# Kernel tuning notes

Measured on AMD Instinct MI355X. Metric: run time of the kernel, lower is better.

The kernel has to match this reference:

```python
import jax, jax.numpy as jnp
import numpy as np
from jax import lax

D_MODEL = 1024
D_STATE = 128
D_CONV = 4
EXPAND = 2
HEADDIM = 64
D_INNER = EXPAND * D_MODEL          # 2048
NHEADS = D_INNER // HEADDIM         # 32
D_IN_PROJ = 2 * D_INNER + 2 * D_STATE + NHEADS  # 4384 (z, xBC, dt)
CONV_CH = D_INNER + 2 * D_STATE     # 2304
CHUNK = 128
EPS = 1e-5
BATCH, SEQ = 2, 2048


def silu(x):
    return x * jax.nn.sigmoid(x)


def rmsnorm(x, w):
    return x * lax.rsqrt(jnp.mean(x * x, axis=-1, keepdims=True) + EPS) * w


def segsum(a):
    # a: (b,h,c,q) -> (b,h,c,q,q); [i,j] = sum_{j<k<=i} a_k, -inf above diag
    q = a.shape[-1]
    cs = jnp.cumsum(a, axis=-1)
    seg = cs[..., :, None] - cs[..., None, :]
    mask = jnp.tril(jnp.ones((q, q), dtype=bool))
    return jnp.where(mask, seg, -jnp.inf)


def ssd(xh, dt, A, B, C):
    # xh: (b,l,h,p), dt: (b,l,h), A: (h,), B,C: (b,l,n). Chunked SSD scan.
    b, l, h, p = xh.shape
    n = B.shape[-1]
    c = l // CHUNK
    X = (xh * dt[..., None]).reshape(b, c, CHUNK, h, p)
    Adt = (A * dt).reshape(b, c, CHUNK, h).transpose(0, 3, 1, 2)  # (b,h,c,q)
    Bc = B.reshape(b, c, CHUNK, n)
    Cc = C.reshape(b, c, CHUNK, n)
    Acs = jnp.cumsum(Adt, axis=-1)
    L = jnp.exp(segsum(Adt))  # (b,h,c,q,q) causal decay within chunk
    Y_diag = jnp.einsum('bcln,bcsn,bhcls,bcshp->bclhp', Cc, Bc, L, X)
    decay_states = jnp.exp(Acs[..., -1:] - Acs)
    states = jnp.einsum('bcln,bhcl,bclhp->bchpn', Bc, decay_states, X)
    chunk_decay = jnp.exp(Acs[..., -1])  # (b,h,c)

    def step(s, inp):
        st, cd = inp
        return s * cd[:, :, None, None] + st, s

    init = jnp.zeros((b, h, p, n), dtype=xh.dtype)
    _, prev = lax.scan(step, init,
                       (states.transpose(1, 0, 2, 3, 4), chunk_decay.transpose(2, 0, 1)))
    # prev: (c,b,h,p,n) = state at start of each chunk
    Y_off = jnp.einsum('bcln,cbhpn,bhcl->bclhp', Cc, prev, jnp.exp(Acs))
    return (Y_diag + Y_off).reshape(b, l, h, p)


def mamba2(x, in_w, conv_w, conv_b, dt_bias, A_log, D, gnorm_w, out_w):
    b, l, _ = x.shape
    zxbcdt = x @ in_w.T  # (b,l,D_IN_PROJ)
    z = zxbcdt[..., :D_INNER]
    xBC = zxbcdt[..., D_INNER:D_INNER + CONV_CH]
    dt = jax.nn.softplus(zxbcdt[..., D_INNER + CONV_CH:] + dt_bias)  # (b,l,h)
    # causal depthwise conv1d
    xp = jnp.pad(xBC, ((0, 0), (D_CONV - 1, 0), (0, 0)))
    conv = sum(xp[:, k:k + l, :] * conv_w[:, k] for k in range(D_CONV)) + conv_b
    xBC = silu(conv)
    xs = xBC[..., :D_INNER]
    B = xBC[..., D_INNER:D_INNER + D_STATE]
    C = xBC[..., D_INNER + D_STATE:]
    A = -jnp.exp(A_log)
    xh = xs.reshape(b, l, NHEADS, HEADDIM)
    y = ssd(xh, dt, A, B, C) + xh * D[None, None, :, None]
    y = y.reshape(b, l, D_INNER)
    y = rmsnorm(y * silu(z), gnorm_w)  # RMSNormGated
    return y @ out_w.T


def setup_inputs() -> dict:
    key = jax.random.key(0)
    ks = jax.random.split(key, 24)
    d = {}
    d['x'] = jax.random.normal(ks[0], (BATCH, SEQ, D_MODEL), dtype=jnp.float32)
    d['norm_w'] = jnp.ones((D_MODEL,), jnp.float32)
    d['out_w_blk'] = jax.random.normal(ks[1], (D_MODEL, 2 * D_MODEL), jnp.float32) * 0.02
    d['out_b_blk'] = jnp.zeros((D_MODEL,), jnp.float32)
    for i, pfx in enumerate(['f_', 'b_']):
        o = 2 + i * 10
        d[pfx + 'in_w'] = jax.random.normal(ks[o], (D_IN_PROJ, D_MODEL), jnp.float32) * 0.02
        d[pfx + 'conv_w'] = jax.random.normal(ks[o + 1], (CONV_CH, D_CONV), jnp.float32) * 0.2
        d[pfx + 'conv_b'] = jnp.zeros((CONV_CH,), jnp.float32)
        d[pfx + 'dt_bias'] = jax.random.normal(ks[o + 2], (NHEADS,), jnp.float32) * 0.1
        d[pfx + 'A_log'] = jnp.log(jax.random.uniform(ks[o + 3], (NHEADS,), jnp.float32, 1.0, 16.0))
        d[pfx + 'D'] = jnp.ones((NHEADS,), jnp.float32)
        d[pfx + 'gnorm_w'] = jnp.ones((D_INNER,), jnp.float32)
        d[pfx + 'out_w'] = jax.random.normal(ks[o + 4], (D_MODEL, D_INNER), jnp.float32) * 0.02
    return d


def reference(x, norm_w, out_w_blk, out_b_blk,
              f_in_w, f_conv_w, f_conv_b, f_dt_bias, f_A_log, f_D, f_gnorm_w, f_out_w,
              b_in_w, b_conv_w, b_conv_b, b_dt_bias, b_A_log, b_D, b_gnorm_w, b_out_w):
    xn = rmsnorm(x, norm_w)
    y_fwd = mamba2(xn, f_in_w, f_conv_w, f_conv_b, f_dt_bias, f_A_log, f_D, f_gnorm_w, f_out_w)
    y_bwd = jnp.flip(
        mamba2(jnp.flip(xn, axis=1), b_in_w, b_conv_w, b_conv_b, b_dt_bias, b_A_log, b_D, b_gnorm_w, b_out_w),
        axis=1)
    out = jnp.concatenate([y_fwd, y_bwd], axis=-1) @ out_w_blk.T + out_b_blk
    return x + out
```

## Files before the change

kernel.cpp:

```cpp
#include <hip/hip_runtime.h>
#include <hip/hip_bf16.h>
#include <math.h>

#define BATCH 2
#define SEQL 2048
#define T 4096
#define DMODEL 1024
#define DINNER 2048
#define DSTATE 128
#define NH 32
#define HD 64
#define DPROJ2 4352
#define CONVCH 2304
#define NCH 16
#define CHUNK 128
#define EPS 1e-5f

#define N_INW ((size_t)DPROJ2 * DMODEL)
#define N_OUTW ((size_t)DMODEL * DINNER)
#define N_ST ((size_t)BATCH * NCH * NH * HD * DSTATE)
#define F2B_BLOCKS 10752
#define TW_BLOCKS 1024

typedef unsigned short u16;
typedef __bf16 bf16x8 __attribute__((ext_vector_type(8)));
typedef float f32x4 __attribute__((ext_vector_type(4)));

__device__ __forceinline__ u16 f2b(float f) {
    union { float f; unsigned u; } v; v.f = f;
    unsigned r = v.u + 0x7fffu + ((v.u >> 16) & 1u);
    return (u16)(r >> 16);
}
__device__ __forceinline__ float b2f(u16 b) {
    union { unsigned u; float f; } v; v.u = ((unsigned)b) << 16;
    return v.f;
}
__device__ __forceinline__ int flipseq(int r) {
    return (r & ~(SEQL - 1)) | ((SEQL - 1) - (r & (SEQL - 1)));
}
__device__ __forceinline__ void gload16(const u16* g, u16* l) {
    __builtin_amdgcn_global_load_lds(
        (const __attribute__((address_space(1))) void*)g,
        (__attribute__((address_space(3))) void*)l, 16, 0, 0);
}

__device__ __forceinline__ float blockReduceSum(float v) {
    __shared__ float red_[4];
    for (int off = 32; off > 0; off >>= 1) v += __shfl_down(v, off);
    int lane = threadIdx.x & 63, wid = threadIdx.x >> 6;
    if (lane == 0) red_[wid] = v;
    __syncthreads();
    if (threadIdx.x == 0) {
        float s = 0.f;
        int nw = blockDim.x >> 6;
        for (int i = 0; i < nw; ++i) s += red_[i];
        red_[0] = s;
    }
    __syncthreads();
    return red_[0];
}

__global__ __launch_bounds__(256) void k_rmsnorm(
    const float* __restrict__ x, const float* __restrict__ w,
    u16* __restrict__ outb)
{
    int row = blockIdx.x;
    const float* xr = x + (size_t)row * DMODEL;
    float ss = 0.f;
    for (int i = threadIdx.x; i < DMODEL; i += 256) { float v = xr[i]; ss += v * v; }
    float tot = blockReduceSum(ss);
    float sc = rsqrtf(tot / DMODEL + EPS);
    for (int i = threadIdx.x; i < DMODEL; i += 256)
        outb[(size_t)row * DMODEL + i] = f2b(xr[i] * sc * w[i]);
}

__global__ __launch_bounds__(256) void k_wprep(
    const float* __restrict__ f_in_w, const float* __restrict__ b_in_w,
    const float* __restrict__ out_w_blk,
    const float* __restrict__ f_out_w, const float* __restrict__ b_out_w,
    u16* __restrict__ d_inwb, u16* __restrict__ d_owbb, u16* __restrict__ d_fowT)
{
    __shared__ u16 t[64][65];
    int bid = blockIdx.x;
    if (bid < F2B_BLOCKS) {
        size_t i = ((size_t)bid * 256 + threadIdx.x) * 4;
        const float* s; u16* d; size_t off;
        if (i < 2 * N_INW) {
            int dir = i >= N_INW;
            off = i - (size_t)dir * N_INW;
            s = dir ? b_in_w : f_in_w; d = d_inwb + (size_t)dir * N_INW;
        } else {
            off = i - 2 * N_INW;
            if (off >= N_OUTW) return;
            s = out_w_blk; d = d_owbb;
        }
        float4 v = *(const float4*)(s + off);
        ushort4 o;
        o.x = f2b(v.x); o.y = f2b(v.y); o.z = f2b(v.z); o.w = f2b(v.w);
        *(ushort4*)(d + off) = o;
        return;
    }
    int b2 = bid - F2B_BLOCKS;
    int dir = b2 >> 9;
    int rem = b2 & 511;
    int c0 = (rem & 31) * 64, e0 = (rem >> 5) * 64;
    const float* src = dir ? b_out_w : f_out_w;
    u16* d = d_fowT + (size_t)dir * N_OUTW;
    for (int i = threadIdx.x; i < 64 * 16; i += 256) {
        int el = i >> 4, c4 = (i & 15) * 4;
        float4 v = *(const float4*)(src + (size_t)(e0 + el) * DINNER + c0 + c4);
        t[c4 + 0][el] = f2b(v.x); t[c4 + 1][el] = f2b(v.y);
        t[c4 + 2][el] = f2b(v.z); t[c4 + 3][el] = f2b(v.w);
    }
    __syncthreads();
    for (int i = threadIdx.x; i < 64 * 16; i += 256) {
        int cl = i >> 4, e4 = (i & 15) * 4;
        ushort4 o;
        o.x = t[cl][e4]; o.y = t[cl][e4 + 1]; o.z = t[cl][e4 + 2]; o.w = t[cl][e4 + 3];
        *(ushort4*)(d + (size_t)(c0 + cl) * DMODEL + e0 + e4) = o;
    }
}

__global__ __launch_bounds__(256, 4) void k_mm_in(
    const u16* __restrict__ A, const u16* __restrict__ W0,
    u16* __restrict__ zb0, u16* __restrict__ xbcraw0)
{
    const int K = DMODEL;
    int dir = blockIdx.z;
    const u16* W = W0 + (size_t)dir * N_INW;
    int m0 = blockIdx.x * 128, n0 = blockIdx.y * 128;

    u16* Cout;
    int ldcc, nbase;
    if (n0 < DINNER) {
        Cout = zb0 + (size_t)dir * T * DINNER;
        ldcc = DINNER;
        nbase = n0;
    } else {
        Cout = xbcraw0 + (size_t)dir * T * CONVCH;
        ldcc = CONVCH;
        nbase = n0 - DINNER;
    }

    __shared__ u16 As[2 * 128 * 32];
    __shared__ u16 Bs[2 * 128 * 32];
    int tid = threadIdx.x;
    int lane = tid & 63;
    int wrow = ((tid >> 6) & 1) * 64, wcol = (tid >> 7) * 64;

    int srow = tid >> 2, skof = (tid & 3) * 8;
    int ar1 = m0 + srow, ar2 = ar1 + 64;
    if (dir) { ar1 = flipseq(ar1); ar2 = flipseq(ar2); }
    const u16* ga1 = A + (size_t)ar1 * K + skof;
    const u16* ga2 = A + (size_t)ar2 * K + skof;
    const u16* gb1 = W + (size_t)(n0 + srow) * K + skof;
    const u16* gb2 = gb1 + (size_t)64 * K;
    u16* la1 = As + tid * 8;
    u16* la2 = As + 2048 + tid * 8;
    u16* lb1 = Bs + tid * 8;
    u16* lb2 = Bs + 2048 + tid * 8;

    int aoff[4], boff[4];
    #pragma unroll
    for (int i = 0; i < 4; ++i) {
        aoff[i] = (wrow + i * 16 + (lane & 15)) * 32 + ((lane >> 4) * 8);
        boff[i] = (wcol + i * 16 + (lane & 15)) * 32 + ((lane >> 4) * 8);
    }

    f32x4 acc[4][4] = {};
    for (int kt = 0; kt < K; kt += 64) {
        gload16(ga1, la1);        gload16(ga2, la2);
        gload16(ga1 + 32, la1 + 4096); gload16(ga2 + 32, la2 + 4096);
        gload16(gb1, lb1);        gload16(gb2, lb2);
        gload16(gb1 + 32, lb1 + 4096); gload16(gb2 + 32, lb2 + 4096);
        ga1 += 64; ga2 += 64; gb1 += 64; gb2 += 64;
        __syncthreads();
        #pragma unroll
        for (int ks = 0; ks < 2; ++ks) {
            bf16x8 af[4], bfv[4];
            #pragma unroll
            for (int i = 0; i < 4; ++i) af[i] = *(const bf16x8*)(As + ks * 4096 + aoff[i]);
            #pragma unroll
            for (int j = 0; j < 4; ++j) bfv[j] = *(const bf16x8*)(Bs + ks * 4096 + boff[j]);
            #pragma unroll
            for (int i = 0; i < 4; ++i)
                #pragma unroll
                for (int j = 0; j < 4; ++j)
                    acc[i][j] = __builtin_amdgcn_mfma_f32_16x16x32_bf16(af[i], bfv[j], acc[i][j], 0, 0, 0);
        }
        __syncthreads();
    }

    int rbase = m0 + wrow + ((lane >> 4) << 2);
    int cbase = nbase + wcol + (lane & 15);
    #pragma unroll
    for (int i = 0; i < 4; ++i)
        #pragma unroll
        for (int j = 0; j < 4; ++j)
            #pragma unroll
            for (int r = 0; r < 4; ++r)
                Cout[(size_t)(rbase + i * 16 + r) * ldcc + cbase + j * 16] = f2b(acc[i][j][r]);
}

__global__ __launch_bounds__(256) void k_mm64(
    const u16* __restrict__ A, size_t astride, int lda,
    const u16* __restrict__ W, size_t wstride, int K,
    u16* __restrict__ Cb, int ldc, int coffStride)
{
    int dir = blockIdx.z;
    A += (size_t)dir * astride;
    W += (size_t)dir * wstride;
    int coff = dir * coffStride;

    __shared__ u16 As[2 * 64 * 32];
    __shared__ u16 Bs[2 * 64 * 32];
    int tid = threadIdx.x;
    int lane = tid & 63;
    int w = tid >> 6;
    int m0 = blockIdx.y * 64, n0 = blockIdx.x * 64;
    int wrow = (w & 1) * 32, wcol = (w >> 1) * 32;

    int srow = tid >> 2, skof = (tid & 3) * 8;
    const u16* ga = A + (size_t)(m0 + srow) * lda + skof;
    const u16* gb = W + (size_t)(n0 + srow) * K + skof;
    u16* la = As + tid * 8;
    u16* lb = Bs + tid * 8;

    int aoff[2], boff[2];
    #pragma unroll
    for (int i = 0; i < 2; ++i) {
        aoff[i] = (wrow + i * 16 + (lane & 15)) * 32 + ((lane >> 4) * 8);
        boff[i] = (wcol + i * 16 + (lane & 15)) * 32 + ((lane >> 4) * 8);
    }

    f32x4 acc[2][2] = {};
    for (int kt = 0; kt < K; kt += 64) {
        gload16(ga, la);      gload16(ga + 32, la + 2048);
        gload16(gb, lb);      gload16(gb + 32, lb + 2048);
        ga += 64; gb += 64;
        __syncthreads();
        #pragma unroll
        for (int ks = 0; ks < 2; ++ks) {
            bf16x8 af[2], bfv[2];
            #pragma unroll
            for (int i = 0; i < 2; ++i) af[i] = *(const bf16x8*)(As + ks * 2048 + aoff[i]);
            #pragma unroll
            for (int j = 0; j < 2; ++j) bfv[j] = *(const bf16x8*)(Bs + ks * 2048 + boff[j]);
            #pragma unroll
            for (int i = 0; i < 2; ++i)
                #pragma unroll
                for (int j = 0; j < 2; ++j)
                    acc[i][j] = __builtin_amdgcn_mfma_f32_16x16x32_bf16(af[i], bfv[j], acc[i][j], 0, 0, 0);
        }
        __syncthreads();
    }

    int rbase = m0 + wrow + ((lane >> 4) << 2);
    int cbase = n0 + wcol + (lane & 15);
    #pragma unroll
    for (int i = 0; i < 2; ++i)
        #pragma unroll
        for (int j = 0; j < 2; ++j)
            #pragma unroll
            for (int r = 0; r < 4; ++r)
                Cb[(size_t)(rbase + i * 16 + r) * ldc + coff + cbase + j * 16] = f2b(acc[i][j][r]);
}

__global__ __launch_bounds__(256) void k_mm_fin(
    const u16* __restrict__ A1, const u16* __restrict__ A2,
    const u16* __restrict__ W,
    float* __restrict__ out, const float* __restrict__ bias,
    const float* __restrict__ resid)
{
    __shared__ u16 As[4 * 64 * 32];
    __shared__ u16 Bs[4 * 64 * 32];
    int tid = threadIdx.x;
    int lane = tid & 63;
    int w = tid >> 6;
    int m0 = blockIdx.y * 64, n0 = blockIdx.x * 64;
    int wrow = (w & 1) * 32, wcol = (w >> 1) * 32;

    int srow = tid >> 2, skof = (tid & 3) * 8;
    const u16* ga1 = A1 + (size_t)(m0 + srow) * DINNER + skof;
    const u16* ga2 = A2 + (size_t)flipseq(m0 + srow) * DINNER + skof;
    const u16* gb1 = W + (size_t)(n0 + srow) * 4096 + skof;
    const u16* gb2 = gb1 + 2048;
    u16* la = As + tid * 8;
    u16* lb = Bs + tid * 8;

    int aoff[2], boff[2];
    #pragma unroll
    for (int i = 0; i < 2; ++i) {
        aoff[i] = (wrow + i * 16 + (lane & 15)) * 32 + ((lane >> 4) * 8);
        boff[i] = (wcol + i * 16 + (lane & 15)) * 32 + ((lane >> 4) * 8);
    }

    f32x4 acc[2][2] = {};
    for (int kt = 0; kt < DINNER; kt += 64) {
        gload16(ga1, la);       gload16(ga1 + 32, la + 2048);
        gload16(ga2, la + 4096); gload16(ga2 + 32, la + 6144);
        gload16(gb1, lb);       gload16(gb1 + 32, lb + 2048);
        gload16(gb2, lb + 4096); gload16(gb2 + 32, lb + 6144);
        ga1 += 64; ga2 += 64; gb1 += 64; gb2 += 64;
        __syncthreads();
        #pragma unroll
        for (int half = 0; half < 2; ++half) {
            #pragma unroll
            for (int ks = 0; ks < 2; ++ks) {
                bf16x8 af[2], bfv[2];
                #pragma unroll
                for (int i = 0; i < 2; ++i)
                    af[i] = *(const bf16x8*)(As + half * 4096 + ks * 2048 + aoff[i]);
                #pragma unroll
                for (int j = 0; j < 2; ++j)
                    bfv[j] = *(const bf16x8*)(Bs + half * 4096 + ks * 2048 + boff[j]);
                #pragma unroll
                for (int i = 0; i < 2; ++i)
                    #pragma unroll
                    for (int j = 0; j < 2; ++j)
                        acc[i][j] = __builtin_amdgcn_mfma_f32_16x16x32_bf16(af[i], bfv[j], acc[i][j], 0, 0, 0);
            }
        }
        __syncthreads();
    }

    int rbase = m0 + wrow + ((lane >> 4) << 2);
    int cbase = n0 + wcol + (lane & 15);
    #pragma unroll
    for (int i = 0; i < 2; ++i)
        #pragma unroll
        for (int j = 0; j < 2; ++j)
            #pragma unroll
            for (int r = 0; r < 4; ++r) {
                int row = rbase + i * 16 + r, col = cbase + j * 16;
                out[(size_t)row * DMODEL + col] =
                    acc[i][j][r] + bias[col] + resid[(size_t)row * DMODEL + col];
            }
}

__global__ __launch_bounds__(256) void k_dt2(
    const u16* __restrict__ xnb,
    const float* __restrict__ inw_f, const float* __restrict__ inw_b,
    const float* __restrict__ dtb_f, const float* __restrict__ dtb_b,
    float* __restrict__ dt)
{
    int dir = blockIdx.z;
    const float* wbase = dir ? inw_b : inw_f;
    const float* dtbia = dir ? dtb_b : dtb_f;
    float* dtp = dt + (size_t)dir * T * NH;

    int r0 = blockIdx.x * 4;
    __shared__ float xs[4][1024];
    int tid = threadIdx.x;
    #pragma unroll
    for (int rr = 0; rr < 4; ++rr) {
        int src = dir ? flipseq(r0 + rr) : (r0 + rr);
        ushort4 v = *(const ushort4*)(xnb + (size_t)src * DMODEL + tid * 4);
        xs[rr][tid * 4 + 0] = b2f(v.x); xs[rr][tid * 4 + 1] = b2f(v.y);
        xs[rr][tid * 4 + 2] = b2f(v.z); xs[rr][tid * 4 + 3] = b2f(v.w);
    }
    __syncthreads();
    int h = tid >> 3, part = tid & 7;
    const float* w = wbase + (size_t)(DPROJ2 + h) * DMODEL;
    float a0 = 0.f, a1 = 0.f, a2 = 0.f, a3 = 0.f;
    for (int kk = 0; kk < 128; ++kk) {
        int k = part + (kk << 3);
        float wv = w[k];
        a0 += xs[0][k] * wv; a1 += xs[1][k] * wv;
        a2 += xs[2][k] * wv; a3 += xs[3][k] * wv;
    }
    #pragma unroll
    for (int off = 4; off > 0; off >>= 1) {
        a0 += __shfl_down(a0, off, 8); a1 += __shfl_down(a1, off, 8);
        a2 += __shfl_down(a2, off, 8); a3 += __shfl_down(a3, off, 8);
    }
    if (part == 0) {
        float bsh = dtbia[h];
        float vv[4] = {a0, a1, a2, a3};
        #pragma unroll
        for (int rr = 0; rr < 4; ++rr) {
            float v = vv[rr] + bsh;
            dtp[(size_t)(r0 + rr) * NH + h] = (v > 20.f) ? v : log1pf(expf(v));
        }
    }
}

__global__ void k_conv(const u16* __restrict__ xraw0,
                       const float* __restrict__ cw_f, const float* __restrict__ cw_b,
                       const float* __restrict__ cb_f, const float* __restrict__ cb_b,
                       const float* __restrict__ dt0,
                       u16* __restrict__ xbcb0, u16* __restrict__ xdtb0)
{
    int dir = blockIdx.z;
    const u16* xraw = xraw0 + (size_t)dir * T * CONVCH;
    const float* cw = dir ? cw_b : cw_f;
    const float* cb = dir ? cb_b : cb_f;
    const float* dt = dt0 + (size_t)dir * T * NH;
    u16* xbcb = xbcb0 + (size_t)dir * T * CONVCH;
    u16* xdtb = xdtb0 + (size_t)dir * T * DINNER;

    int idx = blockIdx.x * blockDim.x + threadIdx.x;
    if (idx >= (T / 4) * (CONVCH / 8)) return;
    int r4 = idx / (CONVCH / 8);
    int c8 = (idx - r4 * (CONVCH / 8)) * 8;
    int r0 = r4 * 4;
    int t0 = r0 & (SEQL - 1);

    float4 cwv[8];
    #pragma unroll
    for (int j = 0; j < 8; ++j) cwv[j] = *(const float4*)(cw + (size_t)(c8 + j) * 4);
    float acc[4][8];
    {
        float4 c0 = *(const float4*)(cb + c8);
        float4 c1 = *(const float4*)(cb + c8 + 4);
        #pragma unroll
        for (int i = 0; i < 4; ++i) {
            acc[i][0] = c0.x; acc[i][1] = c0.y; acc[i][2] = c0.z; acc[i][3] = c0.w;
            acc[i][4] = c1.x; acc[i][5] = c1.y; acc[i][6] = c1.z; acc[i][7] = c1.w;
        }
    }
    #pragma unroll
    for (int s = 0; s < 7; ++s) {
        int tt = t0 - 3 + s;
        if (tt < 0) continue;
        const u16* src = xraw + (size_t)(r0 - 3 + s) * CONVCH + c8;
        ushort4 v0 = *(const ushort4*)src;
        ushort4 v1 = *(const ushort4*)(src + 4);
        float xv[8] = {b2f(v0.x), b2f(v0.y), b2f(v0.z), b2f(v0.w),
                       b2f(v1.x), b2f(v1.y), b2f(v1.z), b2f(v1.w)};
        #pragma unroll
        for (int i = 0; i < 4; ++i) {
            if (i <= s && i >= s - 3) {
                const int j = s - i;
                #pragma unroll
                for (int ch = 0; ch < 8; ++ch) {
                    float wv = (j == 0) ? cwv[ch].x : (j == 1) ? cwv[ch].y
                             : (j == 2) ? cwv[ch].z : cwv[ch].w;
                    acc[i][ch] += xv[ch] * wv;
                }
            }
        }
    }
    #pragma unroll
    for (int i = 0; i < 4; ++i) {
        int r = r0 + i;
        float sgl[8];
        #pragma unroll
        for (int ch = 0; ch < 8; ++ch) sgl[ch] = acc[i][ch] / (1.f + __expf(-acc[i][ch]));
        ushort4 o0, o1;
        o0.x = f2b(sgl[0]); o0.y = f2b(sgl[1]); o0.z = f2b(sgl[2]); o0.w = f2b(sgl[3]);
        o1.x = f2b(sgl[4]); o1.y = f2b(sgl[5]); o1.z = f2b(sgl[6]); o1.w = f2b(sgl[7]);
        *(ushort4*)(xbcb + (size_t)r * CONVCH + c8) = o0;
        *(ushort4*)(xbcb + (size_t)r * CONVCH + c8 + 4) = o1;
        if (c8 < DINNER) {
            float dv = dt[(size_t)r * NH + (c8 >> 6)];
            ushort4 d0, d1;
            d0.x = f2b(sgl[0] * dv); d0.y = f2b(sgl[1] * dv);
            d0.z = f2b(sgl[2] * dv); d0.w = f2b(sgl[3] * dv);
            d1.x = f2b(sgl[4] * dv); d1.y = f2b(sgl[5] * dv);
            d1.z = f2b(sgl[6] * dv); d1.w = f2b(sgl[7] * dv);
            *(ushort4*)(xdtb + (size_t)r * DINNER + c8) = d0;
            *(ushort4*)(xdtb + (size_t)r * DINNER + c8 + 4) = d1;
        }
    }
}

#define LDW 136
__global__ __launch_bounds__(256) void k_states(
    const u16* __restrict__ xbcb0, const u16* __restrict__ xdtb0,
    const float* __restrict__ dt0,
    const float* __restrict__ Alog_f, const float* __restrict__ Alog_b,
    float* __restrict__ acs0, float* __restrict__ cd0, u16* __restrict__ st0)
{
    int dir = blockIdx.z;
    const u16* xbcb = xbcb0 + (size_t)dir * T * CONVCH;
    const u16* xdtb = xdtb0 + (size_t)dir * T * DINNER;
    const float* dt = dt0 + (size_t)dir * T * NH;
    const float* A_log = dir ? Alog_b : Alog_f;
    float* acs = acs0 + (size_t)dir * BATCH * NH * NCH * CHUNK;
    float* cd = cd0 + (size_t)dir * BATCH * NH * NCH;
    u16* st = st0 + (size_t)dir * N_ST;

    __shared__ u16 Bt[128 * LDW];
    __shared__ u16 Xt[64 * LDW];
    __shared__ float cs[128];
    __shared__ float dec_s[128];
    int tid = threadIdx.x;
    int lane = tid & 63;
    int w = tid >> 6;
    int h = blockIdx.x & 31;
    int bc = blockIdx.x >> 5;
    int c = bc & 15, b = bc >> 4;
    int row0 = b * SEQL + c * CHUNK;

    if (tid < 128) {
        float Ah = -expf(A_log[h]);
        cs[tid] = Ah * dt[(size_t)(row0 + tid) * NH + h];
    }
    for (int i = tid; i < 128 * 16; i += 256) {
        int l = i >> 4, pg = (i & 15) * 4;
        ushort4 v = *(const ushort4*)(xdtb + (size_t)(row0 + l) * DINNER + h * HD + pg);
        Xt[(pg + 0) * LDW + l] = v.x; Xt[(pg + 1) * LDW + l] = v.y;
        Xt[(pg + 2) * LDW + l] = v.z; Xt[(pg + 3) * LDW + l] = v.w;
    }
    __syncthreads();
    for (int off = 1; off < 128; off <<= 1) {
        float tval = 0.f;
        if (tid < 128 && tid >= off) tval = cs[tid - off];
        __syncthreads();
        if (tid < 128) cs[tid] += tval;
        __syncthreads();
    }
    size_t abase = ((size_t)(b * NH + h) * NCH + c) << 7;
    if (tid < 128) acs[abase + tid] = cs[tid];
    float a_last = cs[127];
    if (tid == 127) cd[(b * NH + h) * NCH + c] = expf(a_last);
    if (tid < 128) dec_s[tid] = __expf(a_last - cs[tid]);
    __syncthreads();
    for (int i = tid; i < 128 * 32; i += 256) {
        int l = i >> 5, ng = (i & 31) * 4;
        ushort4 v = *(const ushort4*)(xbcb + (size_t)(row0 + l) * CONVCH + DINNER + ng);
        float d = dec_s[l];
        Bt[(ng + 0) * LDW + l] = f2b(b2f(v.x) * d);
        Bt[(ng + 1) * LDW + l] = f2b(b2f(v.y) * d);
        Bt[(ng + 2) * LDW + l] = f2b(b2f(v.z) * d);
        Bt[(ng + 3) * LDW + l] = f2b(b2f(v.w) * d);
    }
    __syncthreads();
    f32x4 tacc[8] = {};
    for (int kk = 0; kk < 4; ++kk) {
        bf16x8 afs = *(const bf16x8*)(Xt + (w * 16 + (lane & 15)) * LDW
                                      + kk * 32 + (lane >> 4) * 8);
        #pragma unroll
        for (int j = 0; j < 8; ++j) {
            bf16x8 bfs = *(const bf16x8*)(Bt + (j * 16 + (lane & 15)) * LDW
                                          + kk * 32 + (lane >> 4) * 8);
            tacc[j] = __builtin_amdgcn_mfma_f32_16x16x32_bf16(afs, bfs, tacc[j], 0, 0, 0);
        }
    }
    size_t sb = (size_t)blockIdx.x * (HD * DSTATE);
    #pragma unroll
    for (int j = 0; j < 8; ++j)
        #pragma unroll
        for (int r = 0; r < 4; ++r) {
            int p = w * 16 + (lane >> 4) * 4 + r;
            int n = j * 16 + (lane & 15);
            st[sb + (size_t)p * DSTATE + n] = f2b(tacc[j][r]);
        }
}

__global__ void k_scan(u16* __restrict__ st0, const float* __restrict__ cd0)
{
    int i = blockIdx.x * blockDim.x + threadIdx.x;
    if (i >= 2 * BATCH * NH * HD * DSTATE) return;
    int dir = i >> 19;
    int j = i & ((1 << 19) - 1);
    u16* st = st0 + (size_t)dir * N_ST;
    const float* cd = cd0 + (size_t)dir * BATCH * NH * NCH;
    int n = j & 127;
    int rest = j >> 7;
    int p = rest & 63; rest >>= 6;
    int h = rest & 31;
    int b = rest >> 5;
    float s = 0.f;
    for (int c = 0; c < NCH; ++c) {
        size_t idx = ((size_t)((b * NCH + c) * NH + h) * HD + p) * DSTATE + n;
        float v = b2f(st[idx]);
        st[idx] = f2b(s);
        s = s * cd[(b * NH + h) * NCH + c] + v;
    }
}

__global__ __launch_bounds__(256) void k_chunk(
    const u16* __restrict__ xbcb0, const u16* __restrict__ xdtb0,
    const float* __restrict__ acs0, const u16* __restrict__ prev0,
    const float* __restrict__ D_f, const float* __restrict__ D_b,
    u16* __restrict__ y0)
{
    int dir = blockIdx.z;
    const u16* xbcb = xbcb0 + (size_t)dir * T * CONVCH;
    const u16* xdtb = xdtb0 + (size_t)dir * T * DINNER;
    const float* acs = acs0 + (size_t)dir * BATCH * NH * NCH * CHUNK;
    const u16* prev = prev0 + (size_t)dir * N_ST;
    const float* Dp = dir ? D_b : D_f;
    u16* y = y0 + (size_t)dir * T * DINNER;

    __shared__ u16 S0[128 * LDW];
    __shared__ u16 Xt[64 * LDW];
    __shared__ float acs_s[128];
    int tid = threadIdx.x;
    int lane = tid & 63;
    int w = tid >> 6;
    int h = blockIdx.x & 31;
    int bc = blockIdx.x >> 5;
    int c = bc & 15, b = bc >> 4;
    int row0 = b * SEQL + c * CHUNK;

    if (tid < 128)
        acs_s[tid] = acs[(((size_t)(b * NH + h) * NCH + c) << 7) + tid];
    for (int i = tid; i < 128 * 16; i += 256) {
        int s = i >> 4, m8 = (i & 15) * 8;
        *(uint4*)(S0 + s * LDW + m8) =
            *(const uint4*)(xbcb + (size_t)(row0 + s) * CONVCH + DINNER + m8);
    }
    for (int i = tid; i < 128 * 16; i += 256) {
        int l = i >> 4, pg = (i & 15) * 4;
        ushort4 v = *(const ushort4*)(xdtb + (size_t)(row0 + l) * DINNER + h * HD + pg);
        Xt[(pg + 0) * LDW + l] = v.x; Xt[(pg + 1) * LDW + l] = v.y;
        Xt[(pg + 2) * LDW + l] = v.z; Xt[(pg + 3) * LDW + l] = v.w;
    }
    __syncthreads();

    int wrow = (w & 1) * 64, wcol = (w >> 1) * 64;
    const u16* cbase = xbcb + (size_t)row0 * CONVCH + DINNER + DSTATE;
    f32x4 sacc[4][4] = {};
    for (int kk = 0; kk < 4; ++kk) {
        bf16x8 af[4], bfr[4];
        #pragma unroll
        for (int i = 0; i < 4; ++i)
            af[i] = *(const bf16x8*)(cbase + (size_t)(wrow + i * 16 + (lane & 15)) * CONVCH
                                     + kk * 32 + (lane >> 4) * 8);
        #pragma unroll
        for (int j = 0; j < 4; ++j)
            bfr[j] = *(const bf16x8*)(S0 + (wcol + j * 16 + (lane & 15)) * LDW
                                      + kk * 32 + (lane >> 4) * 8);
        #pragma unroll
        for (int i = 0; i < 4; ++i)
            #pragma unroll
            for (int j = 0; j < 4; ++j)
                if (wcol + j * 16 <= wrow + i * 16 + 15)
                    sacc[i][j] = __builtin_amdgcn_mfma_f32_16x16x32_bf16(af[i], bfr[j], sacc[i][j], 0, 0, 0);
    }
    __syncthreads();
    #pragma unroll
    for (int i = 0; i < 4; ++i)
        #pragma unroll
        for (int j = 0; j < 4; ++j) {
            int s = wcol + j * 16 + (lane & 15);
            #pragma unroll
            for (int r = 0; r < 4; ++r) {
                int l = wrow + i * 16 + (lane >> 4) * 4 + r;
                float v = (s <= l) ? sacc[i][j][r] * __expf(acs_s[l] - acs_s[s]) : 0.f;
                S0[l * LDW + s] = f2b(v);
            }
        }
    __syncthreads();
    f32x4 yacc[2][4] = {};
    for (int kk = 0; kk < 4; ++kk) {
        bf16x8 af[2], bfr[4];
        #pragma unroll
        for (int i = 0; i < 2; ++i)
            af[i] = *(const bf16x8*)(S0 + (w * 32 + i * 16 + (lane & 15)) * LDW
                                     + kk * 32 + (lane >> 4) * 8);
        #pragma unroll
        for (int j = 0; j < 4; ++j)
            bfr[j] = *(const bf16x8*)(Xt + (j * 16 + (lane & 15)) * LDW
                                      + kk * 32 + (lane >> 4) * 8);
        #pragma unroll
        for (int i = 0; i < 2; ++i)
            #pragma unroll
            for (int j = 0; j < 4; ++j)
                yacc[i][j] = __builtin_amdgcn_mfma_f32_16x16x32_bf16(af[i], bfr[j], yacc[i][j], 0, 0, 0);
    }
    __syncthreads();
    size_t sb = (size_t)blockIdx.x * (HD * DSTATE);
    for (int i = tid; i < 64 * 16; i += 256) {
        int p = i >> 4, m8 = (i & 15) * 8;
        *(uint4*)(S0 + p * LDW + m8) = *(const uint4*)(prev + sb + (size_t)p * DSTATE + m8);
    }
    __syncthreads();
    f32x4 oacc[2][4] = {};
    for (int kk = 0; kk < 4; ++kk) {
        bf16x8 af[2], bfr[4];
        #pragma unroll
        for (int i = 0; i < 2; ++i)
            af[i] = *(const bf16x8*)(cbase + (size_t)(w * 32 + i * 16 + (lane & 15)) * CONVCH
                                     + kk * 32 + (lane >> 4) * 8);
        #pragma unroll
        for (int j = 0; j < 4; ++j)
            bfr[j] = *(const bf16x8*)(S0 + (j * 16 + (lane & 15)) * LDW
                                      + kk * 32 + (lane >> 4) * 8);
        #pragma unroll
        for (int i = 0; i < 2; ++i)
            #pragma unroll
            for (int j = 0; j < 4; ++j)
                oacc[i][j] = __builtin_amdgcn_mfma_f32_16x16x32_bf16(af[i], bfr[j], oacc[i][j], 0, 0, 0);
    }
    float Dh = Dp[h];
    #pragma unroll
    for (int i = 0; i < 2; ++i)
        #pragma unroll
        for (int j = 0; j < 4; ++j)
            #pragma unroll
            for (int r = 0; r < 4; ++r) {
                int l = w * 32 + i * 16 + (lane >> 4) * 4 + r;
                int p = j * 16 + (lane & 15);
                float val = yacc[i][j][r] + __expf(acs_s[l]) * oacc[i][j][r]
                          + b2f(xbcb[(size_t)(row0 + l) * CONVCH + h * HD + p]) * Dh;
                y[(size_t)(row0 + l) * DINNER + h * HD + p] = f2b(val);
            }
}

__global__ __launch_bounds__(256) void k_gate(
    const u16* __restrict__ y0, const u16* __restrict__ zb0,
    const float* __restrict__ gw_f, const float* __restrict__ gw_b,
    u16* __restrict__ out0)
{
    int dir = blockIdx.z;
    const u16* y = y0 + (size_t)dir * T * DINNER;
    const u16* zb = zb0 + (size_t)dir * T * DINNER;
    const float* gw = dir ? gw_b : gw_f;
    u16* out = out0 + (size_t)dir * T * DINNER;

    int r = blockIdx.x;
    int tid = threadIdx.x;
    float tv[8];
    float ss = 0.f;
    #pragma unroll
    for (int it = 0; it < 2; ++it) {
        int i = (it * 256 + tid) * 4;
        ushort4 yv = *(const ushort4*)(y + (size_t)r * DINNER + i);
        ushort4 zv = *(const ushort4*)(zb + (size_t)r * DINNER + i);
        float z0 = b2f(zv.x), z1 = b2f(zv.y), z2 = b2f(zv.z), z3 = b2f(zv.w);
        float t0 = b2f(yv.x) * (z0 / (1.f + __expf(-z0)));
        float t1 = b2f(yv.y) * (z1 / (1.f + __expf(-z1)));
        float t2 = b2f(yv.z) * (z2 / (1.f + __expf(-z2)));
        float t3 = b2f(yv.w) * (z3 / (1.f + __expf(-z3)));
        tv[it * 4 + 0] = t0; tv[it * 4 + 1] = t1; tv[it * 4 + 2] = t2; tv[it * 4 + 3] = t3;
        ss += t0 * t0 + t1 * t1 + t2 * t2 + t3 * t3;
    }
    float tot = blockReduceSum(ss);
    float sc = rsqrtf(tot / DINNER + EPS);
    #pragma unroll
    for (int it = 0; it < 2; ++it) {
        int i = (it * 256 + tid) * 4;
        ushort4 o;
        o.x = f2b(tv[it * 4 + 0] * sc * gw[i]);
        o.y = f2b(tv[it * 4 + 1] * sc * gw[i + 1]);
        o.z = f2b(tv[it * 4 + 2] * sc * gw[i + 2]);
        o.w = f2b(tv[it * 4 + 3] * sc * gw[i + 3]);
        *(ushort4*)(out + (size_t)r * DINNER + i) = o;
    }
}

extern "C" void kernel_launch(void* const* d_in, const int* in_sizes, int n_in,
                              void* d_out, int out_size, void* d_ws, size_t ws_size,
                              hipStream_t stream)
{
    const float* x         = (const float*)d_in[0];
    const float* norm_w    = (const float*)d_in[1];
    const float* out_w_blk = (const float*)d_in[2];
    const float* out_b_blk = (const float*)d_in[3];
    const float* f_in_w    = (const float*)d_in[4];
    const float* f_conv_w  = (const float*)d_in[5];
    const float* f_conv_b  = (const float*)d_in[6];
    const float* f_dt_bias = (const float*)d_in[7];
    const float* f_A_log   = (const float*)d_in[8];
    const float* f_D       = (const float*)d_in[9];
    const float* f_gnorm_w = (const float*)d_in[10];
    const float* f_out_w   = (const float*)d_in[11];
    const float* b_in_w    = (const float*)d_in[12];
    const float* b_conv_w  = (const float*)d_in[13];
    const float* b_conv_b  = (const float*)d_in[14];
    const float* b_dt_bias = (const float*)d_in[15];
    const float* b_A_log   = (const float*)d_in[16];
    const float* b_D       = (const float*)d_in[17];
    const float* b_gnorm_w = (const float*)d_in[18];
    const float* b_out_w   = (const float*)d_in[19];
    float* out = (float*)d_out;

    char* ws = (char*)d_ws;
    u16*  xnb    = (u16*)ws;   ws += (size_t)T * DMODEL * 2;
    u16*  zb     = (u16*)ws;   ws += (size_t)2 * T * DINNER * 2;
    u16*  xbcraw = (u16*)ws;   ws += (size_t)2 * T * CONVCH * 2;
    u16*  xbcb   = (u16*)ws;   ws += (size_t)2 * T * CONVCH * 2;
    u16*  xdtb   = (u16*)ws;   ws += (size_t)2 * T * DINNER * 2;
    float* dtb   = (float*)ws; ws += (size_t)2 * T * NH * 4;
    float* acs   = (float*)ws; ws += (size_t)2 * BATCH * NH * NCH * CHUNK * 4;
    float* cd    = (float*)ws; ws += (size_t)2 * BATCH * NH * NCH * 4;
    u16*  stb    = (u16*)ws;   ws += (size_t)2 * N_ST * 2;
    u16*  inwb   = (u16*)ws;   ws += (size_t)2 * N_INW * 2;
    u16*  fowT2  = (u16*)ws;   ws += (size_t)2 * N_OUTW * 2;
    u16*  owbb   = (u16*)ws;   ws += (size_t)N_OUTW * 2;
    u16*  yb16  = xbcraw;
    u16*  ybb   = xdtb;
    u16*  Mcomb = xbcb;

    k_rmsnorm<<<T, 256, 0, stream>>>(x, norm_w, xnb);
    k_wprep<<<F2B_BLOCKS + TW_BLOCKS, 256, 0, stream>>>(
        f_in_w, b_in_w, out_w_blk, f_out_w, b_out_w, inwb, owbb, fowT2);

    {
        dim3 g(T / 128, DPROJ2 / 128, 2);
        k_mm_in<<<g, 256, 0, stream>>>(xnb, inwb, zb, xbcraw);
    }
    {
        dim3 g(T / 4, 1, 2);
        k_dt2<<<g, 256, 0, stream>>>(xnb, f_in_w, b_in_w, f_dt_bias, b_dt_bias, dtb);
    }
    {
        dim3 g(((T / 4) * (CONVCH / 8) + 255) / 256, 1, 2);
        k_conv<<<g, 256, 0, stream>>>(xbcraw, f_conv_w, b_conv_w, f_conv_b, b_conv_b,
                                      dtb, xbcb, xdtb);
    }
    {
        dim3 g(BATCH * NCH * NH, 1, 2);
        k_states<<<g, 256, 0, stream>>>(xbcb, xdtb, dtb, f_A_log, b_A_log, acs, cd, stb);
    }
    k_scan<<<(2 * BATCH * NH * HD * DSTATE) / 256, 256, 0, stream>>>(stb, cd);
    {
        dim3 g(BATCH * NCH * NH, 1, 2);
        k_chunk<<<g, 256, 0, stream>>>(xbcb, xdtb, acs, stb, f_D, b_D, yb16);
    }
    {
        dim3 g(T, 1, 2);
        k_gate<<<g, 256, 0, stream>>>(yb16, zb, f_gnorm_w, b_gnorm_w, ybb);
    }
    {
        dim3 g(DINNER / 64, DMODEL / 64, 2);
        k_mm64<<<g, 256, 0, stream>>>(owbb, (size_t)DMODEL, DINNER,
                                      fowT2, N_OUTW, DMODEL,
                                      Mcomb, 2 * DINNER, DINNER);
    }
    {
        dim3 g(DMODEL / 64, T / 64, 1);
        k_mm_fin<<<g, 256, 0, stream>>>(ybb, ybb + (size_t)T * DINNER, Mcomb,
                                        out, out_b_blk, x);
    }
}
```

Measured before the change: 513.2 us.

## Rewrite input projection GEMM with 256x256 tiles, 8 waves and swizzled pipelined LDS

Replaces the 128x128, 4-wave input-projection GEMM with a 256x256-tile, 512-thread kernel. It uses XOR-swizzled LDS layout, staggered prefetching of the next A and B k-tiles interleaved with MFMA groups, explicit waitcnt/barrier control and setprio around the MFMAs. The goal is higher data reuse per LDS byte and better overlap of global loads with matrix math. In exchange it uses 128KB LDS and fewer, larger blocks, which can cause wave quantization across CUs.

```diff
diff --git a/kernel.cpp b/kernel.cpp
--- a/kernel.cpp
+++ b/kernel.cpp
@@ -44,6 +44,8 @@
         (__attribute__((address_space(3))) void*)l, 16, 0, 0);
 }
 
+#define FENCE asm volatile("" ::: "memory")
+
 __device__ __forceinline__ float blockReduceSum(float v) {
     __shared__ float red_[4];
     for (int off = 32; off > 0; off >>= 1) v += __shfl_down(v, off);
@@ -121,17 +123,16 @@
     }
 }
 
-__global__ __launch_bounds__(256, 4) void k_mm_in(
+__global__ __launch_bounds__(512, 2) void k_mm_in8(
     const u16* __restrict__ A, const u16* __restrict__ W0,
     u16* __restrict__ zb0, u16* __restrict__ xbcraw0)
 {
-    const int K = DMODEL;
+    __shared__ u16 lds_[8 * 8192];
     int dir = blockIdx.z;
     const u16* W = W0 + (size_t)dir * N_INW;
-    int m0 = blockIdx.x * 128, n0 = blockIdx.y * 128;
-
-    u16* Cout;
-    int ldcc, nbase;
+    int m0 = blockIdx.x * 256, n0 = blockIdx.y * 256;
+
+    u16* Cout; int ldcc, nbase;
     if (n0 < DINNER) {
         Cout = zb0 + (size_t)dir * T * DINNER;
         ldcc = DINNER;
@@ -142,64 +143,108 @@
         nbase = n0 - DINNER;
     }
 
-    __shared__ u16 As[2 * 128 * 32];
-    __shared__ u16 Bs[2 * 128 * 32];
     int tid = threadIdx.x;
     int lane = tid & 63;
-    int wrow = ((tid >> 6) & 1) * 64, wcol = (tid >> 7) * 64;
-
-    int srow = tid >> 2, skof = (tid & 3) * 8;
-    int ar1 = m0 + srow, ar2 = ar1 + 64;
-    if (dir) { ar1 = flipseq(ar1); ar2 = flipseq(ar2); }
-    const u16* ga1 = A + (size_t)ar1 * K + skof;
-    const u16* ga2 = A + (size_t)ar2 * K + skof;
-    const u16* gb1 = W + (size_t)(n0 + srow) * K + skof;
-    const u16* gb2 = gb1 + (size_t)64 * K;
-    u16* la1 = As + tid * 8;
-    u16* la2 = As + 2048 + tid * 8;
-    u16* lb1 = Bs + tid * 8;
-    u16* lb2 = Bs + 2048 + tid * 8;
-
-    int aoff[4], boff[4];
-    #pragma unroll
-    for (int i = 0; i < 4; ++i) {
-        aoff[i] = (wrow + i * 16 + (lane & 15)) * 32 + ((lane >> 4) * 8);
-        boff[i] = (wcol + i * 16 + (lane & 15)) * 32 + ((lane >> 4) * 8);
-    }
-
-    f32x4 acc[4][4] = {};
-    for (int kt = 0; kt < K; kt += 64) {
-        gload16(ga1, la1);        gload16(ga2, la2);
-        gload16(ga1 + 32, la1 + 4096); gload16(ga2 + 32, la2 + 4096);
-        gload16(gb1, lb1);        gload16(gb2, lb2);
-        gload16(gb1 + 32, lb1 + 4096); gload16(gb2 + 32, lb2 + 4096);
-        ga1 += 64; ga2 += 64; gb1 += 64; gb2 += 64;
-        __syncthreads();
-        #pragma unroll
-        for (int ks = 0; ks < 2; ++ks) {
-            bf16x8 af[4], bfv[4];
-            #pragma unroll
-            for (int i = 0; i < 4; ++i) af[i] = *(const bf16x8*)(As + ks * 4096 + aoff[i]);
-            #pragma unroll
-            for (int j = 0; j < 4; ++j) bfv[j] = *(const bf16x8*)(Bs + ks * 4096 + boff[j]);
-            #pragma unroll
-            for (int i = 0; i < 4; ++i)
+    int w = tid >> 6;
+    int wm = w >> 2;
+    int wn = w & 3;
+    int l15 = lane & 15;
+    int gsw0 = (((lane >> 4) ^ (lane & 7)) << 3);
+    int gsw1 = (((4 + (lane >> 4)) ^ (lane & 7)) << 3);
+
+    const u16* pA[2][2];
+    const u16* pB[2][2];
+    int swz = ((lane & 7) ^ (lane >> 3)) << 3;
+    #pragma unroll
+    for (int h = 0; h < 2; ++h)
+        #pragma unroll
+        for (int c = 0; c < 2; ++c) {
+            int rl = (w * 2 + c) * 8 + (lane >> 3);
+            int grow = m0 + h * 128 + rl;
+            if (dir) grow = flipseq(grow);
+            pA[h][c] = A + (size_t)grow * DMODEL + swz;
+            pB[h][c] = W + (size_t)(n0 + h * 128 + rl) * DMODEL + swz;
+        }
+    int dst0 = (w * 2 + 0) * 512 + lane * 8;
+    int dst1 = (w * 2 + 1) * 512 + lane * 8;
+
+#define STAGE_A(t_, h_) do { \
+        gload16(pA[h_][0] + (t_) * 64, lds_ + (((t_) & 1) * 4 + (h_)) * 8192 + dst0); \
+        gload16(pA[h_][1] + (t_) * 64, lds_ + (((t_) & 1) * 4 + (h_)) * 8192 + dst1); \
+    } while (0)
+#define STAGE_B(t_, h_) do { \
+        gload16(pB[h_][0] + (t_) * 64, lds_ + (((t_) & 1) * 4 + 2 + (h_)) * 8192 + dst0); \
+        gload16(pB[h_][1] + (t_) * 64, lds_ + (((t_) & 1) * 4 + 2 + (h_)) * 8192 + dst1); \
+    } while (0)
+
+    f32x4 acc[8][4] = {};
+    bf16x8 bfv[4][2];
+
+    STAGE_A(0, 0); STAGE_A(0, 1); STAGE_B(0, 0); STAGE_B(0, 1);
+    FENCE;
+    STAGE_B(1, 0); STAGE_B(1, 1);
+    asm volatile("s_waitcnt vmcnt(4)" ::: "memory");
+    __builtin_amdgcn_s_barrier();
+    FENCE;
+
+    for (int kt = 0; kt < 16; ++kt) {
+        int d = kt & 1;
+        const u16* Ab = lds_ + (d * 4 + wm) * 8192;
+        const u16* Bb = lds_ + (d * 4 + 2 + (wn >> 1)) * 8192;
+        int nrow0 = (wn & 1) * 64;
+        #pragma unroll
+        for (int q = 0; q < 4; ++q) {
+            if (q == 0) {
                 #pragma unroll
-                for (int j = 0; j < 4; ++j)
-                    acc[i][j] = __builtin_amdgcn_mfma_f32_16x16x32_bf16(af[i], bfv[j], acc[i][j], 0, 0, 0);
-        }
-        __syncthreads();
-    }
-
-    int rbase = m0 + wrow + ((lane >> 4) << 2);
-    int cbase = nbase + wcol + (lane & 15);
-    #pragma unroll
-    for (int i = 0; i < 4; ++i)
+                for (int j = 0; j < 4; ++j) {
+                    const u16* bp = Bb + (nrow0 + j * 16 + l15) * 64;
+                    bfv[j][0] = *(const bf16x8*)(bp + gsw0);
+                    bfv[j][1] = *(const bf16x8*)(bp + gsw1);
+                }
+            }
+            const u16* ap0 = Ab + ((q * 2 + 0) * 16 + l15) * 64;
+            const u16* ap1 = Ab + ((q * 2 + 1) * 16 + l15) * 64;
+            bf16x8 a0k0 = *(const bf16x8*)(ap0 + gsw0);
+            bf16x8 a0k1 = *(const bf16x8*)(ap0 + gsw1);
+            bf16x8 a1k0 = *(const bf16x8*)(ap1 + gsw0);
+            bf16x8 a1k1 = *(const bf16x8*)(ap1 + gsw1);
+            if (q == 0)      { if (kt < 15) STAGE_A(kt + 1, 0); }
+            else if (q == 1) { if (kt < 15) STAGE_A(kt + 1, 1); }
+            else if (q == 2) { if (kt < 14) STAGE_B(kt + 2, 0); }
+            else             { if (kt < 14) STAGE_B(kt + 2, 1); }
+            FENCE;
+            __builtin_amdgcn_s_barrier();
+            asm volatile("s_waitcnt lgkmcnt(0)" ::: "memory");
+            __builtin_amdgcn_s_setprio(1);
+            #pragma unroll
+            for (int j = 0; j < 4; ++j) {
+                acc[q * 2 + 0][j] = __builtin_amdgcn_mfma_f32_16x16x32_bf16(a0k0, bfv[j][0], acc[q * 2 + 0][j], 0, 0, 0);
+                acc[q * 2 + 0][j] = __builtin_amdgcn_mfma_f32_16x16x32_bf16(a0k1, bfv[j][1], acc[q * 2 + 0][j], 0, 0, 0);
+                acc[q * 2 + 1][j] = __builtin_amdgcn_mfma_f32_16x16x32_bf16(a1k0, bfv[j][0], acc[q * 2 + 1][j], 0, 0, 0);
+                acc[q * 2 + 1][j] = __builtin_amdgcn_mfma_f32_16x16x32_bf16(a1k1, bfv[j][1], acc[q * 2 + 1][j], 0, 0, 0);
+            }
+            __builtin_amdgcn_s_setprio(0);
+            if (q == 3) {
+                if (kt < 14)       asm volatile("s_waitcnt vmcnt(4)" ::: "memory");
+                else if (kt == 14) asm volatile("s_waitcnt vmcnt(0)" ::: "memory");
+            }
+            FENCE;
+            __builtin_amdgcn_s_barrier();
+            FENCE;
+        }
+    }
+#undef STAGE_A
+#undef STAGE_B
+
+    int rb = m0 + wm * 128 + ((lane >> 4) << 2);
+    int cb = nbase + wn * 64 + l15;
+    #pragma unroll
+    for (int i = 0; i < 8; ++i)
         #pragma unroll
         for (int j = 0; j < 4; ++j)
             #pragma unroll
             for (int r = 0; r < 4; ++r)
-                Cout[(size_t)(rbase + i * 16 + r) * ldcc + cbase + j * 16] = f2b(acc[i][j][r]);
+                Cout[(size_t)(rb + i * 16 + r) * ldcc + cb + j * 16] = f2b(acc[i][j][r]);
 }
 
 __global__ __launch_bounds__(256) void k_mm64(
@@ -791,8 +836,8 @@
         f_in_w, b_in_w, out_w_blk, f_out_w, b_out_w, inwb, owbb, fowT2);
 
     {
-        dim3 g(T / 128, DPROJ2 / 128, 2);
-        k_mm_in<<<g, 256, 0, stream>>>(xnb, inwb, zb, xbcraw);
+        dim3 g(T / 256, DPROJ2 / 256, 2);
+        k_mm_in8<<<g, 512, 0, stream>>>(xnb, inwb, zb, xbcraw);
     }
     {
         dim3 g(T / 4, 1, 2);
```

New measurement: 527.6 us. 1.03x slower.
